# Kernel optimization log

Measured on AMD Instinct MI355X. Metric: run time of the kernel, lower is better.

## Reference

```python
import jax, jax.numpy as jnp
import numpy as np

E = 192; Q = 48; H = 3; HD = Q // H  # per-branch embed 48, 3 heads of 16
CONV_CH = 4; K = 15; PAD = K // 2


def layer_norm(x, g, b, eps=1e-6):
    m = jnp.mean(x, axis=-1, keepdims=True)
    v = jnp.mean((x - m) ** 2, axis=-1, keepdims=True)
    return (x - m) * jax.lax.rsqrt(v + eps) * g + b


def mha(x, w_in, b_in, w_o, b_o):
    # x: [B,S,48]; torch nn.MultiheadAttention math (dropout=eval/identity)
    B, S, _ = x.shape
    qkv = x @ w_in.T + b_in                      # [B,S,144]
    q, k, v = jnp.split(qkv, 3, axis=-1)
    q = q.reshape(B, S, H, HD)
    k = k.reshape(B, S, H, HD)
    v = v.reshape(B, S, H, HD)
    scores = jnp.einsum('bqhd,bkhd->bhqk', q, k) / jnp.sqrt(jnp.float32(HD))
    attn = jax.nn.softmax(scores, axis=-1)
    out = jnp.einsum('bhqk,bkhd->bqhd', attn, v).reshape(B, S, Q)
    return out @ w_o.T + b_o


def light_conv(x96, conv_w):
    # x96: [B,S,96] -> view(-1, 4, 96), depthwise conv1d (k=15, pad=7), view back
    B, S, W = x96.shape
    r = x96.reshape(-1, CONV_CH, W)              # [B*S/... wait: B*S*96/(4*96)=B*S/4? No: reshape(-1,4,96) => [B*S, ...]
    y = jax.lax.conv_general_dilated(
        r, conv_w, window_strides=(1,), padding=[(PAD, PAD)],
        dimension_numbers=('NCH', 'OIH', 'NCH'), feature_group_count=CONV_CH)
    return y.reshape(B, S, W)


def setup_inputs() -> dict:
    key = jax.random.key(0)
    ks = jax.random.split(key, 16)
    sc = 0.05
    d = {
        'x': jax.random.normal(ks[0], (128, 512, E), dtype=jnp.float32),
        'ln1_g': jnp.ones((E,), jnp.float32), 'ln1_b': jnp.zeros((E,), jnp.float32),
        'acc_wqkv': jax.random.normal(ks[1], (3 * Q, Q), jnp.float32) * sc,
        'acc_bqkv': jnp.zeros((3 * Q,), jnp.float32),
        'acc_wo': jax.random.normal(ks[2], (Q, Q), jnp.float32) * sc,
        'acc_bo': jnp.zeros((Q,), jnp.float32),
        'gyro_wqkv': jax.random.normal(ks[3], (3 * Q, Q), jnp.float32) * sc,
        'gyro_bqkv': jnp.zeros((3 * Q,), jnp.float32),
        'gyro_wo': jax.random.normal(ks[4], (Q, Q), jnp.float32) * sc,
        'gyro_bo': jnp.zeros((Q,), jnp.float32),
        'conv_w': jax.random.normal(ks[5], (CONV_CH, 1, K), jnp.float32) * sc,
        'ln2_g': jnp.ones((E,), jnp.float32), 'ln2_b': jnp.zeros((E,), jnp.float32),
        'w1': jax.random.normal(ks[6], (2 * E, E), jnp.float32) * sc,
        'b1': jnp.zeros((2 * E,), jnp.float32),
        'w2': jax.random.normal(ks[7], (E, 2 * E), jnp.float32) * sc,
        'b2': jnp.zeros((E,), jnp.float32),
    }
    return d


def reference(x, ln1_g, ln1_b, acc_wqkv, acc_bqkv, acc_wo, acc_bo,
              gyro_wqkv, gyro_bqkv, gyro_wo, gyro_bo, conv_w,
              ln2_g, ln2_b, w1, b1, w2, b2):
    xn = layer_norm(x, ln1_g, ln1_b)
    x_conv = light_conv(xn[:, :, 48:144], conv_w)
    x_acc = mha(xn[:, :, 0:48], acc_wqkv, acc_bqkv, acc_wo, acc_bo)
    x_gyro = mha(xn[:, :, 96:144], gyro_wqkv, gyro_bqkv, gyro_wo, gyro_bo)
    xcat = jnp.concatenate([x_acc, x_conv, x_gyro], axis=2)
    x1 = xcat + x
    tt = layer_norm(x1, ln2_g, ln2_b)
    tt = jax.nn.relu(tt @ w1.T + b1)
    tt = jax.nn.relu(tt @ w2.T + b2)
    return x1 + tt
```

## Files before the change

### kernel.cpp

```cpp
#include <hip/hip_runtime.h>
#include <stdint.h>

typedef unsigned short u16;
typedef short bf16x8 __attribute__((ext_vector_type(8)));
typedef float f32x4 __attribute__((ext_vector_type(4)));
typedef float f32x16 __attribute__((ext_vector_type(16)));
typedef uint32_t u32x4 __attribute__((ext_vector_type(4)));

#define NB   128
#define SEQ  512
#define EMB  192
#define NTOK (NB * SEQ)
#define F1DIM 384
#define ATTW 192
#define VTP  520
#define KTS  24
#define XnS  200
#define H1S  392

__device__ __forceinline__ float bf2f(u16 u) {
  union { uint32_t u; float f; } v; v.u = ((uint32_t)u) << 16; return v.f;
}
__device__ __forceinline__ u16 f2bf(float f) {
  union { float f; uint32_t u; } v; v.f = f;
  uint32_t r = v.u + 0x7fffu + ((v.u >> 16) & 1u);
  return (u16)(r >> 16);
}
__device__ __forceinline__ uint32_t pack2bf(float a, float b) {
  return (uint32_t)f2bf(a) | ((uint32_t)f2bf(b) << 16);
}

__global__ __launch_bounds__(256) void pack_kernel(const float* __restrict__ w1,
    const float* __restrict__ w2, const float* __restrict__ wqa,
    const float* __restrict__ wqg, const float* __restrict__ woa,
    const float* __restrict__ wog, u16* __restrict__ w1b, u16* __restrict__ w2b,
    u16* __restrict__ wqp, u16* __restrict__ wop) {
  int idx = (int)blockIdx.x * 256 + (int)threadIdx.x;
  if (idx < 73728) {
    w1b[idx] = f2bf(w1[idx]);
  } else if (idx < 147456) {
    w2b[idx - 73728] = f2bf(w2[idx - 73728]);
  } else if (idx < 165888) {
    int i = idx - 147456;
    int row = i >> 6, k = i & 63;
    float v = 0.0f;
    if (k < 48) v = (row < 144) ? wqa[row * 48 + k] : wqg[(row - 144) * 48 + k];
    wqp[i] = f2bf(v);
  } else if (idx < 172032) {
    int i = idx - 165888;
    int row = i >> 6, k = i & 63;
    float v = 0.0f;
    if (k < 48) v = (row < 48) ? woa[row * 48 + k] : wog[(row - 48) * 48 + k];
    wop[i] = f2bf(v);
  }
}

__global__ __launch_bounds__(256) void ln1_qkv_conv_kernel(
    const float* __restrict__ x, const float* __restrict__ g,
    const float* __restrict__ b, const u16* __restrict__ wq,
    const float* __restrict__ bacc, const float* __restrict__ bgyr,
    const float* __restrict__ cw, u16* __restrict__ qkv,
    u16* __restrict__ att) {
  __shared__ u16 Xn[64 * XnS];
  int bm = (int)blockIdx.x * 64;
  int tid = threadIdx.x;
  int trow = tid >> 2, part = tid & 3;
  int tok = bm + trow;
  const float* xr = x + (size_t)tok * EMB + part * 48;
  float vals[48];
#pragma unroll
  for (int j = 0; j < 48; j += 4) {
    float4 v = *(const float4*)(xr + j);
    vals[j] = v.x; vals[j + 1] = v.y; vals[j + 2] = v.z; vals[j + 3] = v.w;
  }
  float s = 0.0f, s2 = 0.0f;
#pragma unroll
  for (int j = 0; j < 48; j++) { s += vals[j]; s2 += vals[j] * vals[j]; }
  s += __shfl_xor(s, 1); s2 += __shfl_xor(s2, 1);
  s += __shfl_xor(s, 2); s2 += __shfl_xor(s2, 2);
  float mean = s * (1.0f / EMB);
  float var  = s2 * (1.0f / EMB) - mean * mean;
  float rs   = rsqrtf(var + 1e-6f);
  {
    u16* xnrow = Xn + trow * XnS + part * 48;
    const float* gp = g + part * 48;
    const float* bp = b + part * 48;
#pragma unroll
    for (int j = 0; j < 48; j += 2) {
      uint32_t w = pack2bf((vals[j] - mean) * rs * gp[j] + bp[j],
                           (vals[j + 1] - mean) * rs * gp[j + 1] + bp[j + 1]);
      *(uint32_t*)(xnrow + j) = w;
    }
  }
  __syncthreads();
  int wid = tid >> 6, lane = tid & 63;
  int l15 = lane & 15, quad = lane >> 4;
  const u16* arow_l = Xn + (wid * 16 + l15) * XnS;
  f32x4 acc[18] = {};
#pragma unroll
  for (int ks = 0; ks < 2; ks++) {
    int kk = ks * 32;
    bf16x8 af_a = *(const bf16x8*)(arow_l + kk + quad * 8);
    bf16x8 af_g = *(const bf16x8*)(arow_l + 96 + kk + quad * 8);
#pragma unroll
    for (int st = 0; st < 18; st++) {
      bf16x8 bf = *(const bf16x8*)(wq + (size_t)(st * 16 + l15) * 64 + kk + quad * 8);
      acc[st] = __builtin_amdgcn_mfma_f32_16x16x32_bf16(st < 9 ? af_a : af_g,
                                                        bf, acc[st], 0, 0, 0);
    }
  }
#pragma unroll
  for (int st = 0; st < 18; st++) {
    int col = st * 16 + l15;
    int cc = (col < 144) ? col : col - 144;
    float bias = (col < 144) ? bacc[cc] : bgyr[cc];
    float qs = (cc < 48) ? 0.36067376022f : 1.0f;
#pragma unroll
    for (int r = 0; r < 4; r++) {
      int orow = bm + wid * 16 + quad * 4 + r;
      qkv[(size_t)orow * 288 + col] = f2bf((acc[st][r] + bias) * qs);
    }
  }
  {
    int wr = trow & 3;
    float w15[15];
#pragma unroll
    for (int k = 0; k < 15; k++) w15[k] = cw[wr * 15 + k];
    float win[38];
    int base = part * 24 - 7;
#pragma unroll
    for (int i = 0; i < 38; i++) {
      int p = base + i;
      win[i] = (p >= 0 && p < 96) ? bf2f(Xn[trow * XnS + 48 + p]) : 0.0f;
    }
    const float* xres = x + (size_t)tok * EMB + 48 + part * 24;
    u16* orow = att + (size_t)tok * ATTW + 96 + part * 24;
#pragma unroll
    for (int c = 0; c < 24; c += 4) {
      float4 r4 = *(const float4*)(xres + c);
      float o[4];
#pragma unroll
      for (int u = 0; u < 4; u++) {
        float sc = 0.0f;
#pragma unroll
        for (int k = 0; k < 15; k++) sc += win[c + u + k] * w15[k];
        o[u] = sc;
      }
      *(uint32_t*)(orow + c)     = pack2bf(o[0] + r4.x, o[1] + r4.y);
      *(uint32_t*)(orow + c + 2) = pack2bf(o[2] + r4.z, o[3] + r4.w);
    }
  }
}

__global__ __launch_bounds__(256) void attn_kernel(const u16* __restrict__ qkv,
                                                   u16* __restrict__ att) {
  __shared__ u16 Kt[SEQ * KTS];
  __shared__ u16 Vt[17 * VTP];
  int bid = blockIdx.x;
  int hh  = bid % 3;
  int brb = (bid / 3) & 1;
  int b   = bid / 6;
  int tid = threadIdx.x;
  size_t tokbase = (size_t)b * SEQ;
  int qoff = brb * 144 + hh * 16;
  int koff = qoff + 48;
  int voff = qoff + 96;
  for (int r = tid; r < SEQ; r += 256) {
    const u16* src = qkv + (tokbase + r) * 288;
    *(uint4*)(Kt + r * KTS)     = *(const uint4*)(src + koff);
    *(uint4*)(Kt + r * KTS + 8) = *(const uint4*)(src + koff + 8);
    u16 tmp[16];
    *(uint4*)(tmp)     = *(const uint4*)(src + voff);
    *(uint4*)(tmp + 8) = *(const uint4*)(src + voff + 8);
#pragma unroll
    for (int j = 0; j < 16; j++) Vt[j * VTP + r] = tmp[j];
  }
  Vt[16 * VTP + tid]       = 0x3F80;
  Vt[16 * VTP + 256 + tid] = 0x3F80;
  __syncthreads();
  int wave = tid >> 6, lane = tid & 63;
  int q31 = lane & 31, h = lane >> 5;
  int dcl = (q31 < 16) ? q31 : 16;
#pragma unroll 1
  for (int qi = 0; qi < 4; qi++) {
    int qrow = (wave * 4 + qi) * 32 + q31;
    bf16x8 qfrag = *(const bf16x8*)(qkv + (tokbase + qrow) * 288 + qoff + h * 8);
    f32x16 Ot = {};
#pragma unroll 2
    for (int kt = 0; kt < 16; kt++) {
      bf16x8 kfrag = *(const bf16x8*)(Kt + (kt * 32 + q31) * KTS + h * 8);
      f32x16 zc = {};
      f32x16 S = __builtin_amdgcn_mfma_f32_32x32x16_bf16(kfrag, qfrag, zc, 0, 0, 0);
      uint32_t pk[8], swk[8];
#pragma unroll
      for (int i = 0; i < 8; i++) {
        union { float f; uint32_t u; } a0, a1;
        a0.f = exp2f(S[2 * i]);
        a1.f = exp2f(S[2 * i + 1]);
        pk[i] = __builtin_amdgcn_perm(a1.u, a0.u, 0x07060302u);
        swk[i] = (uint32_t)__shfl_xor((int)pk[i], 32);
      }
      u32x4 t1 = { h ? swk[2] : pk[0], h ? swk[3] : pk[1],
                   h ? pk[2]  : swk[0], h ? pk[3]  : swk[1] };
      u32x4 t2 = { h ? swk[6] : pk[4], h ? swk[7] : pk[5],
                   h ? pk[6]  : swk[4], h ? pk[7]  : swk[5] };
      bf16x8 pb1 = __builtin_bit_cast(bf16x8, t1);
      bf16x8 pb2 = __builtin_bit_cast(bf16x8, t2);
      bf16x8 av1 = *(const bf16x8*)(Vt + dcl * VTP + kt * 32 + h * 8);
      bf16x8 av2 = *(const bf16x8*)(Vt + dcl * VTP + kt * 32 + 16 + h * 8);
      Ot = __builtin_amdgcn_mfma_f32_32x32x16_bf16(av1, pb1, Ot, 0, 0, 0);
      Ot = __builtin_amdgcn_mfma_f32_32x32x16_bf16(av2, pb2, Ot, 0, 0, 0);
    }
    float inv = 1.0f / Ot[8];
    u16* orow = att + (tokbase + qrow) * ATTW + brb * 48 + hh * 16 + 4 * h;
    uint2 st0 = { pack2bf(Ot[0] * inv, Ot[1] * inv),
                  pack2bf(Ot[2] * inv, Ot[3] * inv) };
    uint2 st1 = { pack2bf(Ot[4] * inv, Ot[5] * inv),
                  pack2bf(Ot[6] * inv, Ot[7] * inv) };
    *(uint2*)(orow)     = st0;
    *(uint2*)(orow + 8) = st1;
  }
}

__global__ __launch_bounds__(256) void tail_kernel(
    const u16* __restrict__ att, const u16* __restrict__ wo,
    const float* __restrict__ boacc, const float* __restrict__ bogyr,
    const float* __restrict__ x, const float* __restrict__ g2,
    const float* __restrict__ b2v, const u16* __restrict__ w1b,
    const float* __restrict__ b1, const u16* __restrict__ w2b,
    const float* __restrict__ b2, float* __restrict__ out) {
  __shared__ u16 LDSB[32 * XnS + 16 * H1S];
  u16* X1b = LDSB;
  u16* Tn  = LDSB + 16 * XnS;
  u16* H1  = LDSB + 32 * XnS;
  int bm = (int)blockIdx.x * 16;
  int tid = threadIdx.x;
  int wid = tid >> 6, lane = tid & 63;
  int l15 = lane & 15, quad = lane >> 4;

  if (wid == 3) {
    int trow = lane >> 2, p4 = lane & 3;
    const u16* src = att + (size_t)(bm + trow) * ATTW + 96 + p4 * 24;
    u16* dst = X1b + trow * XnS + 48 + p4 * 24;
    *(uint4*)(dst)      = *(const uint4*)(src);
    *(uint4*)(dst + 8)  = *(const uint4*)(src + 8);
    *(uint4*)(dst + 16) = *(const uint4*)(src + 16);
  } else {
    const u16* arow0 = att + (size_t)(bm + l15) * ATTW;
    bf16x8 afA[2], afG[2];
#pragma unroll
    for (int ks = 0; ks < 2; ks++) {
      afA[ks] = *(const bf16x8*)(arow0 + ks * 32 + quad * 8);
      afG[ks] = *(const bf16x8*)(arow0 + 48 + ks * 32 + quad * 8);
    }
    f32x4 acc[2] = {};
#pragma unroll
    for (int s = 0; s < 2; s++) {
      int st = wid * 2 + s;
      int ng = (st >= 3) ? 1 : 0;
#pragma unroll
      for (int ks = 0; ks < 2; ks++) {
        bf16x8 bf = *(const bf16x8*)(wo + (size_t)(st * 16 + l15) * 64 + ks * 32 + quad * 8);
        acc[s] = __builtin_amdgcn_mfma_f32_16x16x32_bf16(ng ? afG[ks] : afA[ks],
                                                         bf, acc[s], 0, 0, 0);
      }
    }
#pragma unroll
    for (int s = 0; s < 2; s++) {
      int st = wid * 2 + s;
      int col = st * 16 + l15;
      float bias = (col < 48) ? boacc[col] : bogyr[col - 48];
      int oc = (col < 48) ? col : col + 96;
#pragma unroll
      for (int r = 0; r < 4; r++) {
        int lrow = quad * 4 + r;
        float v = acc[s][r] + bias + x[(size_t)(bm + lrow) * EMB + oc];
        X1b[lrow * XnS + oc] = f2bf(v);
      }
    }
  }
  __syncthreads();

  {
    int trow = tid >> 4, part = tid & 15;
    const u16* xl = X1b + trow * XnS + part * 12;
    u16 raw[12];
    *(uint2*)(raw)     = *(const uint2*)(xl);
    *(uint2*)(raw + 4) = *(const uint2*)(xl + 4);
    *(uint2*)(raw + 8) = *(const uint2*)(xl + 8);
    float vals[12];
#pragma unroll
    for (int j = 0; j < 12; j++) vals[j] = bf2f(raw[j]);
    float s = 0.0f, s2 = 0.0f;
#pragma unroll
    for (int j = 0; j < 12; j++) { s += vals[j]; s2 += vals[j] * vals[j]; }
    s += __shfl_xor(s, 1); s2 += __shfl_xor(s2, 1);
    s += __shfl_xor(s, 2); s2 += __shfl_xor(s2, 2);
    s += __shfl_xor(s, 4); s2 += __shfl_xor(s2, 4);
    s += __shfl_xor(s, 8); s2 += __shfl_xor(s2, 8);
    float mean = s * (1.0f / EMB);
    float var  = s2 * (1.0f / EMB) - mean * mean;
    float rs   = rsqrtf(var + 1e-6f);
    u16* trp = Tn + trow * XnS + part * 12;
    const float* gp = g2 + part * 12;
    const float* bp = b2v + part * 12;
#pragma unroll
    for (int j = 0; j < 12; j += 2) {
      uint32_t w = pack2bf((vals[j] - mean) * rs * gp[j] + bp[j],
                           (vals[j + 1] - mean) * rs * gp[j + 1] + bp[j + 1]);
      *(uint32_t*)(trp + j) = w;
    }
  }
  __syncthreads();

  f32x4 acc1[6] = {};
#pragma unroll
  for (int kk = 0; kk < 192; kk += 32) {
    bf16x8 a0 = *(const bf16x8*)(Tn + l15 * XnS + kk + quad * 8);
#pragma unroll
    for (int stl = 0; stl < 6; stl++) {
      bf16x8 bf = *(const bf16x8*)(w1b + (size_t)((wid * 6 + stl) * 16 + l15) * EMB + kk + quad * 8);
      acc1[stl] = __builtin_amdgcn_mfma_f32_16x16x32_bf16(a0, bf, acc1[stl], 0, 0, 0);
    }
  }
#pragma unroll
  for (int stl = 0; stl < 6; stl++) {
    int col = (wid * 6 + stl) * 16 + l15;
    float bias = b1[col];
#pragma unroll
    for (int r = 0; r < 4; r++) {
      float v = acc1[stl][r] + bias;
      v = v > 0.0f ? v : 0.0f;
      H1[(quad * 4 + r) * H1S + col] = f2bf(v);
    }
  }
  __syncthreads();

  {
    f32x4 acc2[3] = {};
#pragma unroll
    for (int kk = 0; kk < 384; kk += 32) {
      bf16x8 a0 = *(const bf16x8*)(H1 + l15 * H1S + kk + quad * 8);
#pragma unroll
      for (int stl = 0; stl < 3; stl++) {
        bf16x8 bf = *(const bf16x8*)(w2b + (size_t)((wid * 3 + stl) * 16 + l15) * F1DIM + kk + quad * 8);
        acc2[stl] = __builtin_amdgcn_mfma_f32_16x16x32_bf16(a0, bf, acc2[stl], 0, 0, 0);
      }
    }
#pragma unroll
    for (int stl = 0; stl < 3; stl++) {
      int col = (wid * 3 + stl) * 16 + l15;
      float bias = b2[col];
#pragma unroll
      for (int r = 0; r < 4; r++) {
        int lrow = quad * 4 + r;
        float v = acc2[stl][r] + bias;
        v = v > 0.0f ? v : 0.0f;
        out[(size_t)(bm + lrow) * EMB + col] = v + bf2f(X1b[lrow * XnS + col]);
      }
    }
  }
}

extern "C" void kernel_launch(void* const* d_in, const int* in_sizes, int n_in,
                              void* d_out, int out_size, void* d_ws, size_t ws_size,
                              hipStream_t stream) {
  const float* x         = (const float*)d_in[0];
  const float* ln1_g     = (const float*)d_in[1];
  const float* ln1_b     = (const float*)d_in[2];
  const float* acc_wqkv  = (const float*)d_in[3];
  const float* acc_bqkv  = (const float*)d_in[4];
  const float* acc_wo    = (const float*)d_in[5];
  const float* acc_bo    = (const float*)d_in[6];
  const float* gyro_wqkv = (const float*)d_in[7];
  const float* gyro_bqkv = (const float*)d_in[8];
  const float* gyro_wo   = (const float*)d_in[9];
  const float* gyro_bo   = (const float*)d_in[10];
  const float* conv_w    = (const float*)d_in[11];
  const float* ln2_g     = (const float*)d_in[12];
  const float* ln2_b     = (const float*)d_in[13];
  const float* w1        = (const float*)d_in[14];
  const float* b1        = (const float*)d_in[15];
  const float* w2        = (const float*)d_in[16];
  const float* b2        = (const float*)d_in[17];
  float* out = (float*)d_out;
  char* ws = (char*)d_ws;

  u16* qkvb = (u16*)(ws);
  u16* attb = (u16*)(ws + 37748736);
  u16* w1b  = (u16*)(ws + 62914560);
  u16* w2b  = (u16*)(ws + 63062016);
  u16* wqp  = (u16*)(ws + 63209472);
  u16* wop  = (u16*)(ws + 63246336);

  pack_kernel<<<672, 256, 0, stream>>>(w1, w2, acc_wqkv, gyro_wqkv, acc_wo,
                                       gyro_wo, w1b, w2b, wqp, wop);
  ln1_qkv_conv_kernel<<<NTOK / 64, 256, 0, stream>>>(
      x, ln1_g, ln1_b, wqp, acc_bqkv, gyro_bqkv, conv_w, qkvb, attb);
  attn_kernel<<<NB * 6, 256, 0, stream>>>(qkvb, attb);
  tail_kernel<<<NTOK / 16, 256, 0, stream>>>(
      attb, wop, acc_bo, gyro_bo, x, ln2_g, ln2_b, w1b, b1, w2b, b2, out);
}
```

Measured before the change: 368.8 us.

## Process 32 tokens per tail block with 512 threads to halve weight reloads

The tail kernel now handles 32 rows per block with 8 waves instead of 16 rows with 4 waves. Waves are split into row-halves and column groups, so each weight fragment loaded from global memory serves twice as many tokens. The LN2 output buffer now aliases the H1 buffer, with an extra barrier before H1 is written to keep this safe. The cost is higher per-block LDS and register use, which may lower occupancy, plus one more synchronisation point.

New measurement: 369.6 us. No clear change (+0.2%).

```diff
diff --git a/kernel.cpp b/kernel.cpp
--- a/kernel.cpp
+++ b/kernel.cpp
@@ -222,59 +222,55 @@
   }
 }
 
-__global__ __launch_bounds__(256) void tail_kernel(
+__global__ __launch_bounds__(512) void tail_kernel(
     const u16* __restrict__ att, const u16* __restrict__ wo,
     const float* __restrict__ boacc, const float* __restrict__ bogyr,
     const float* __restrict__ x, const float* __restrict__ g2,
     const float* __restrict__ b2v, const u16* __restrict__ w1b,
     const float* __restrict__ b1, const u16* __restrict__ w2b,
     const float* __restrict__ b2, float* __restrict__ out) {
-  __shared__ u16 LDSB[32 * XnS + 16 * H1S];
+  __shared__ u16 LDSB[32 * XnS + 32 * H1S];
   u16* X1b = LDSB;
-  u16* Tn  = LDSB + 16 * XnS;
+  u16* Tn  = LDSB + 32 * XnS;
   u16* H1  = LDSB + 32 * XnS;
-  int bm = (int)blockIdx.x * 16;
+  int bm = (int)blockIdx.x * 32;
   int tid = threadIdx.x;
   int wid = tid >> 6, lane = tid & 63;
   int l15 = lane & 15, quad = lane >> 4;
 
-  if (wid == 3) {
-    int trow = lane >> 2, p4 = lane & 3;
+  if (wid >= 6) {
+    int trow = (wid - 6) * 16 + (lane >> 2), p4 = lane & 3;
     const u16* src = att + (size_t)(bm + trow) * ATTW + 96 + p4 * 24;
     u16* dst = X1b + trow * XnS + 48 + p4 * 24;
     *(uint4*)(dst)      = *(const uint4*)(src);
     *(uint4*)(dst + 8)  = *(const uint4*)(src + 8);
     *(uint4*)(dst + 16) = *(const uint4*)(src + 16);
   } else {
-    const u16* arow0 = att + (size_t)(bm + l15) * ATTW;
-    bf16x8 afA[2], afG[2];
-#pragma unroll
-    for (int ks = 0; ks < 2; ks++) {
-      afA[ks] = *(const bf16x8*)(arow0 + ks * 32 + quad * 8);
-      afG[ks] = *(const bf16x8*)(arow0 + 48 + ks * 32 + quad * 8);
-    }
+    int st = wid;
+    int ng = (st >= 3) ? 1 : 0;
     f32x4 acc[2] = {};
-#pragma unroll
-    for (int s = 0; s < 2; s++) {
-      int st = wid * 2 + s;
-      int ng = (st >= 3) ? 1 : 0;
+    bf16x8 wf[2];
+#pragma unroll
+    for (int ks = 0; ks < 2; ks++)
+      wf[ks] = *(const bf16x8*)(wo + (size_t)(st * 16 + l15) * 64 + ks * 32 + quad * 8);
+#pragma unroll
+    for (int m = 0; m < 2; m++) {
+      const u16* arow = att + (size_t)(bm + m * 16 + l15) * ATTW + (ng ? 48 : 0);
 #pragma unroll
       for (int ks = 0; ks < 2; ks++) {
-        bf16x8 bf = *(const bf16x8*)(wo + (size_t)(st * 16 + l15) * 64 + ks * 32 + quad * 8);
-        acc[s] = __builtin_amdgcn_mfma_f32_16x16x32_bf16(ng ? afG[ks] : afA[ks],
-                                                         bf, acc[s], 0, 0, 0);
-      }
-    }
-#pragma unroll
-    for (int s = 0; s < 2; s++) {
-      int st = wid * 2 + s;
-      int col = st * 16 + l15;
-      float bias = (col < 48) ? boacc[col] : bogyr[col - 48];
-      int oc = (col < 48) ? col : col + 96;
+        bf16x8 af = *(const bf16x8*)(arow + ks * 32 + quad * 8);
+        acc[m] = __builtin_amdgcn_mfma_f32_16x16x32_bf16(af, wf[ks], acc[m], 0, 0, 0);
+      }
+    }
+    int col = st * 16 + l15;
+    float bias = (col < 48) ? boacc[col] : bogyr[col - 48];
+    int oc = (col < 48) ? col : col + 96;
+#pragma unroll
+    for (int m = 0; m < 2; m++) {
 #pragma unroll
       for (int r = 0; r < 4; r++) {
-        int lrow = quad * 4 + r;
-        float v = acc[s][r] + bias + x[(size_t)(bm + lrow) * EMB + oc];
+        int lrow = m * 16 + quad * 4 + r;
+        float v = acc[m][r] + bias + x[(size_t)(bm + lrow) * EMB + oc];
         X1b[lrow * XnS + oc] = f2bf(v);
       }
     }
@@ -313,25 +309,27 @@
   }
   __syncthreads();
 
+  int mg = wid & 1, ng = wid >> 1;
   f32x4 acc1[6] = {};
 #pragma unroll
   for (int kk = 0; kk < 192; kk += 32) {
-    bf16x8 a0 = *(const bf16x8*)(Tn + l15 * XnS + kk + quad * 8);
+    bf16x8 a0 = *(const bf16x8*)(Tn + (mg * 16 + l15) * XnS + kk + quad * 8);
 #pragma unroll
     for (int stl = 0; stl < 6; stl++) {
-      bf16x8 bf = *(const bf16x8*)(w1b + (size_t)((wid * 6 + stl) * 16 + l15) * EMB + kk + quad * 8);
+      bf16x8 bf = *(const bf16x8*)(w1b + (size_t)((ng * 6 + stl) * 16 + l15) * EMB + kk + quad * 8);
       acc1[stl] = __builtin_amdgcn_mfma_f32_16x16x32_bf16(a0, bf, acc1[stl], 0, 0, 0);
     }
   }
+  __syncthreads();
 #pragma unroll
   for (int stl = 0; stl < 6; stl++) {
-    int col = (wid * 6 + stl) * 16 + l15;
+    int col = (ng * 6 + stl) * 16 + l15;
     float bias = b1[col];
 #pragma unroll
     for (int r = 0; r < 4; r++) {
       float v = acc1[stl][r] + bias;
       v = v > 0.0f ? v : 0.0f;
-      H1[(quad * 4 + r) * H1S + col] = f2bf(v);
+      H1[(mg * 16 + quad * 4 + r) * H1S + col] = f2bf(v);
     }
   }
   __syncthreads();
@@ -340,20 +338,20 @@
     f32x4 acc2[3] = {};
 #pragma unroll
     for (int kk = 0; kk < 384; kk += 32) {
-      bf16x8 a0 = *(const bf16x8*)(H1 + l15 * H1S + kk + quad * 8);
+      bf16x8 a0 = *(const bf16x8*)(H1 + (mg * 16 + l15) * H1S + kk + quad * 8);
 #pragma unroll
       for (int stl = 0; stl < 3; stl++) {
-        bf16x8 bf = *(const bf16x8*)(w2b + (size_t)((wid * 3 + stl) * 16 + l15) * F1DIM + kk + quad * 8);
+        bf16x8 bf = *(const bf16x8*)(w2b + (size_t)((ng * 3 + stl) * 16 + l15) * F1DIM + kk + quad * 8);
         acc2[stl] = __builtin_amdgcn_mfma_f32_16x16x32_bf16(a0, bf, acc2[stl], 0, 0, 0);
       }
     }
 #pragma unroll
     for (int stl = 0; stl < 3; stl++) {
-      int col = (wid * 3 + stl) * 16 + l15;
+      int col = (ng * 3 + stl) * 16 + l15;
       float bias = b2[col];
 #pragma unroll
       for (int r = 0; r < 4; r++) {
-        int lrow = quad * 4 + r;
+        int lrow = mg * 16 + quad * 4 + r;
         float v = acc2[stl][r] + bias;
         v = v > 0.0f ? v : 0.0f;
         out[(size_t)(bm + lrow) * EMB + col] = v + bf2f(X1b[lrow * XnS + col]);
@@ -398,6 +396,6 @@
   ln1_qkv_conv_kernel<<<NTOK / 64, 256, 0, stream>>>(
       x, ln1_g, ln1_b, wqp, acc_bqkv, gyro_bqkv, conv_w, qkvb, attb);
   attn_kernel<<<NB * 6, 256, 0, stream>>>(qkvb, attb);
-  tail_kernel<<<NTOK / 16, 256, 0, stream>>>(
+  tail_kernel<<<NTOK / 32, 512, 0, stream>>>(
       attb, wop, acc_bo, gyro_bo, x, ln2_g, ln2_b, w1b, b1, w2b, b2, out);
 }
```
